# Kernel tuning notes

Measured on AMD Instinct MI355X. Metric: run time of the kernel, lower is better.

The kernel has to match this reference:

```python
import jax, jax.numpy as jnp
import numpy as np

BS, C, H, W = 8, 64, 256, 256
N_MODE_1, N_MODE_2 = 32, 32  # retained modes along H-rfft and W-rfft


def setup_inputs() -> dict:
    key = jax.random.key(0)
    ks = jax.random.split(key, 5)
    ci = co = C // 2
    scale = 1.0 / (C * C)  # module's self.scale flavor; kaiming init approximated by scaled normal
    return {
        "x": jax.random.normal(ks[0], (BS, C, H, W), jnp.float32),
        "w1_re": jax.random.normal(ks[1], (2, ci, co, N_MODE_1), jnp.float32) * 0.05,
        "w1_im": jax.random.normal(ks[2], (2, ci, co, N_MODE_1), jnp.float32) * 0.05,
        "w2_re": jax.random.normal(ks[3], (2, ci, co, N_MODE_2), jnp.float32) * 0.05,
        "w2_im": jax.random.normal(ks[4], (2, ci, co, N_MODE_2), jnp.float32) * 0.05,
    }


def reference(x, w1_re, w1_im, w2_re, w2_im):
    bs, c, h, w = x.shape
    x5 = x.reshape(bs, 2, c // 2, h, w)  # split channels into 2 groups

    # ---- spectral conv along W (dim=-1), weight_2 ----
    w2c = w2_re + 1j * w2_im  # [2, ci, co, n_mode_2]
    x_ft = jnp.fft.rfft(x5, axis=-1, norm="ortho")  # [bs,2,ci,h,w//2+1]
    out_ft = jnp.einsum("bgixy,gioy->bgoxy", x_ft[..., :N_MODE_2], w2c)
    out_ft = jnp.pad(out_ft, ((0, 0), (0, 0), (0, 0), (0, 0), (0, x_ft.shape[-1] - N_MODE_2)))
    x5 = jnp.fft.irfft(out_ft, n=w, axis=-1, norm="ortho")

    # ---- spectral conv along H (dim=-2), weight_1 ----
    w1c = w1_re + 1j * w1_im  # [2, ci, co, n_mode_1]
    x_ft = jnp.fft.rfft(x5, axis=-2, norm="ortho")  # [bs,2,ci,h//2+1,w]
    out_ft = jnp.einsum("bgixy,giox->bgoxy", x_ft[..., :N_MODE_1, :], w1c)
    out_ft = jnp.pad(out_ft, ((0, 0), (0, 0), (0, 0), (0, x_ft.shape[-2] - N_MODE_1), (0, 0)))
    x5 = jnp.fft.irfft(out_ft, n=h, axis=-2, norm="ortho")

    return x5.reshape(bs, c, h, w)
```

## Files before the change

### kernel.cpp

```cpp
#include <hip/hip_runtime.h>
#include <math.h>

#define PI2_256 0.0245436926061702596754894014318f
#define AS 264

typedef __attribute__((ext_vector_type(8))) short short8;
typedef __attribute__((ext_vector_type(4))) float f32x4;

static __device__ __forceinline__ unsigned short f2bf(float f) {
    unsigned int u = __float_as_uint(f);
    u = (u + 0x7FFFu + ((u >> 16) & 1u)) >> 16;
    return (unsigned short)u;
}
static __device__ __forceinline__ float bf2f(unsigned short h) {
    return __uint_as_float(((unsigned int)h) << 16);
}

__global__ __launch_bounds__(256) void init_tab(float* __restrict__ tc, float* __restrict__ ts) {
    int idx = blockIdx.x * 256 + threadIdx.x;
    int k = idx >> 8, n = idx & 255;
    int m = (k * n) & 255;
    float s, c;
    sincosf(PI2_256 * (float)m, &s, &c);
    tc[idx] = c;
    ts[idx] = s;
}

__global__ __launch_bounds__(256) void init_et(unsigned short* __restrict__ Eth,
                                               unsigned short* __restrict__ Etl) {
    int idx = blockIdx.x * 256 + threadIdx.x;
    int n = idx >> 8, w = idx & 255;
    int k = n & 31;
    int m = (k * w) & 255;
    float s, c;
    sincosf(PI2_256 * (float)m, &s, &c);
    float v = (n < 32) ? c : -s;
    unsigned short h = f2bf(v);
    Eth[idx] = h;
    Etl[idx] = f2bf(v - bf2f(h));
}

__global__ __launch_bounds__(256) void w_fwd(const float* __restrict__ x,
                                             const float* __restrict__ w2r,
                                             const float* __restrict__ w2i,
                                             const unsigned short* __restrict__ Eth,
                                             const unsigned short* __restrict__ Etl,
                                             float* __restrict__ Yw) {
    __shared__ __attribute__((aligned(16))) unsigned short Ah[32 * AS];
    __shared__ float XrL[2][32 * 36], XiL[2][32 * 36];

    const int bid = blockIdx.x;
    const int jr  = bid & 127;
    const int g   = (bid >> 7) & 1;
    const int b   = bid >> 8;
    const int t   = threadIdx.x;

    const size_t chan0 = (size_t)(b * 64 + g * 32);

    for (int rr = 0; rr < 2; ++rr) {
        const int xrow = jr * 2 + rr;
        const size_t base = (chan0 * 256 + xrow) * 256;

        {
            const int wq = t & 63, i0 = t >> 6;
            #pragma unroll
            for (int r = 0; r < 8; ++r) {
                const int i = i0 + r * 4;
                const float4 v = *(const float4*)(x + base + (size_t)i * 65536 + wq * 4);
                ushort4 hq;
                hq.x = f2bf(v.x);
                hq.y = f2bf(v.y);
                hq.z = f2bf(v.z);
                hq.w = f2bf(v.w);
                *(ushort4*)(Ah + i * AS + wq * 4) = hq;
            }
        }
        __syncthreads();

        {
            const int l  = t & 63, wv = t >> 6;
            const int lr = l & 15, lk = (l >> 4) * 8;
            f32x4 acc0 = {0.f, 0.f, 0.f, 0.f};
            f32x4 acc1 = {0.f, 0.f, 0.f, 0.f};
            const unsigned short* bhp = Eth + (size_t)(wv * 16 + lr) * 256 + lk;
            const unsigned short* blp = Etl + (size_t)(wv * 16 + lr) * 256 + lk;
            const unsigned short* a0p = Ah + lr * AS + lk;
            const unsigned short* a1p = Ah + (16 + lr) * AS + lk;
            #pragma unroll
            for (int ks = 0; ks < 8; ++ks) {
                const int offg = ks * 32;
                const short8 bh = *(const short8*)(bhp + offg);
                const short8 bl = *(const short8*)(blp + offg);
                const short8 a0 = *(const short8*)(a0p + offg);
                const short8 a1 = *(const short8*)(a1p + offg);
                acc0 = __builtin_amdgcn_mfma_f32_16x16x32_bf16(a0, bh, acc0, 0, 0, 0);
                acc1 = __builtin_amdgcn_mfma_f32_16x16x32_bf16(a1, bh, acc1, 0, 0, 0);
                acc0 = __builtin_amdgcn_mfma_f32_16x16x32_bf16(a0, bl, acc0, 0, 0, 0);
                acc1 = __builtin_amdgcn_mfma_f32_16x16x32_bf16(a1, bl, acc1, 0, 0, 0);
            }
            const int col   = wv * 16 + lr;
            const int rbase = (l >> 4) * 4;
            #pragma unroll
            for (int r = 0; r < 4; ++r) {
                const int row0 = rbase + r;
                const int row1 = 16 + rbase + r;
                const float v0 = acc0[r], v1 = acc1[r];
                if (col < 32) {
                    XrL[rr][row0 * 36 + col] = v0;
                    XrL[rr][row1 * 36 + col] = v1;
                } else {
                    XiL[rr][row0 * 36 + col - 32] = v0;
                    XiL[rr][row1 * 36 + col - 32] = v1;
                }
            }
        }
        __syncthreads();
    }

    {
        const int kq = t & 7, o = t >> 3;
        const int k4 = kq * 4;
        float4 ar0 = {0,0,0,0}, ai0 = {0,0,0,0};
        float4 ar1 = {0,0,0,0}, ai1 = {0,0,0,0};
        const float* wrb = w2r + (size_t)g * 32768 + o * 32 + k4;
        const float* wib = w2i + (size_t)g * 32768 + o * 32 + k4;
        for (int i = 0; i < 32; ++i) {
            const float4 wr  = *(const float4*)(wrb + i * 1024);
            const float4 wi  = *(const float4*)(wib + i * 1024);
            const float4 xr0 = *(const float4*)(&XrL[0][i * 36 + k4]);
            const float4 xi0 = *(const float4*)(&XiL[0][i * 36 + k4]);
            const float4 xr1 = *(const float4*)(&XrL[1][i * 36 + k4]);
            const float4 xi1 = *(const float4*)(&XiL[1][i * 36 + k4]);
            ar0.x += xr0.x * wr.x - xi0.x * wi.x;  ai0.x += xr0.x * wi.x + xi0.x * wr.x;
            ar0.y += xr0.y * wr.y - xi0.y * wi.y;  ai0.y += xr0.y * wi.y + xi0.y * wr.y;
            ar0.z += xr0.z * wr.z - xi0.z * wi.z;  ai0.z += xr0.z * wi.z + xi0.z * wr.z;
            ar0.w += xr0.w * wr.w - xi0.w * wi.w;  ai0.w += xr0.w * wi.w + xi0.w * wr.w;
            ar1.x += xr1.x * wr.x - xi1.x * wi.x;  ai1.x += xr1.x * wi.x + xi1.x * wr.x;
            ar1.y += xr1.y * wr.y - xi1.y * wi.y;  ai1.y += xr1.y * wi.y + xi1.y * wr.y;
            ar1.z += xr1.z * wr.z - xi1.z * wi.z;  ai1.z += xr1.z * wi.z + xi1.z * wr.z;
            ar1.w += xr1.w * wr.w - xi1.w * wi.w;  ai1.w += xr1.w * wi.w + xi1.w * wr.w;
        }
        const float s2 = 2.f / 256.f, s1 = 1.f / 256.f;
        const float s0 = (k4 == 0) ? s1 : s2;
        float* dst0 = Yw + (size_t)((b * 2 + g) * 32 + o) * 16384
                         + (size_t)(jr * 2) * 64 + k4;
        *(float4*)(dst0)           = make_float4(ar0.x * s0, ar0.y * s2, ar0.z * s2, ar0.w * s2);
        *(float4*)(dst0 + 32)      = make_float4(ai0.x * s0, ai0.y * s2, ai0.z * s2, ai0.w * s2);
        *(float4*)(dst0 + 64)      = make_float4(ar1.x * s0, ar1.y * s2, ar1.z * s2, ar1.w * s2);
        *(float4*)(dst0 + 64 + 32) = make_float4(ai1.x * s0, ai1.y * s2, ai1.z * s2, ai1.w * s2);
    }
}

__global__ __launch_bounds__(256) void h_fwd(const float* __restrict__ Yw,
                                             float* __restrict__ Z) {
    __shared__ float YL[256 * 64];
    __shared__ float kC[32], kS[32];
    const int bid = blockIdx.x;
    const int t = threadIdx.x;
    if (t < 32) {
        float s, c; sincosf(PI2_256 * (float)t, &s, &c);
        kC[t] = c; kS[t] = s;
    }
    {
        const float* src = Yw + (size_t)bid * 16384;
        #pragma unroll
        for (int r = 0; r < 16; ++r) {
            const int f = t + r * 256;
            *(float4*)(YL + f * 4) = *(const float4*)(src + f * 4);
        }
    }
    __syncthreads();

    const int hs = t & 1, kg = (t >> 1) & 7, sp = t >> 4;
    const int hb = hs * 64;
    const float sgn = (kg & 1) ? -1.f : 1.f;
    const float4 y0q   = *(const float4*)(YL + sp * 4);
    const float4 y128q = *(const float4*)(YL + 128 * 64 + sp * 4);

    float cA[4], sA[4], cB[4], sB[4], t2[4];
    float xr[4][4], xi[4][4];
    #pragma unroll
    for (int kk = 0; kk < 4; ++kk) {
        const int k = kg + 8 * kk;
        const float cd = kC[k], sd = kS[k];
        t2[kk] = 2.f * cd;
        float cA0, sA0;
        if (hs == 0) { cA0 = 1.f; sA0 = 0.f; }
        else {
            const int km = k & 3;
            cA0 = (km == 0) ? 1.f : (km == 2) ? -1.f : 0.f;
            sA0 = (km == 1) ? 1.f : (km == 3) ? -1.f : 0.f;
        }
        cA[kk] = cA0; sA[kk] = sA0;
        cB[kk] = cA0 * cd + sA0 * sd;
        sB[kk] = sA0 * cd - cA0 * sd;
        #pragma unroll
        for (int j = 0; j < 4; ++j) {
            xr[kk][j] = (hs == 0) ? (sgn * (&y128q.x)[j] - (&y0q.x)[j]) : 0.f;
            xi[kk][j] = 0.f;
        }
    }
    for (int h = hb; h < hb + 64; ++h) {
        const float4 aq = *(const float4*)(YL + h * 64 + sp * 4);
        const float4 mq = *(const float4*)(YL + ((256 - h) & 255) * 64 + sp * 4);
        float ye[4], yo[4];
        #pragma unroll
        for (int j = 0; j < 4; ++j) {
            ye[j] = (&aq.x)[j] + (&mq.x)[j];
            yo[j] = (&aq.x)[j] - (&mq.x)[j];
        }
        #pragma unroll
        for (int kk = 0; kk < 4; ++kk) {
            #pragma unroll
            for (int j = 0; j < 4; ++j) {
                xr[kk][j] += ye[j] * cA[kk];
                xi[kk][j] -= yo[j] * sA[kk];
            }
            const float cn = t2[kk] * cA[kk] - cB[kk]; cB[kk] = cA[kk]; cA[kk] = cn;
            const float sn = t2[kk] * sA[kk] - sB[kk]; sB[kk] = sA[kk]; sA[kk] = sn;
        }
    }
    #pragma unroll
    for (int kk = 0; kk < 4; ++kk)
        #pragma unroll
        for (int j = 0; j < 4; ++j) {
            xr[kk][j] += __shfl_xor(xr[kk][j], 1);
            xi[kk][j] += __shfl_xor(xi[kk][j], 1);
        }
    if (hs == 0) {
        const int o = bid & 31, bg = bid >> 5;
        #pragma unroll
        for (int kk = 0; kk < 4; ++kk) {
            const int k = kg + 8 * kk;
            const size_t zi_ = (((size_t)bg * 32 + k) * 32 + o) * 128 + sp * 4;
            *(float4*)(Z + zi_)      = make_float4(xr[kk][0], xr[kk][1], xr[kk][2], xr[kk][3]);
            *(float4*)(Z + zi_ + 64) = make_float4(xi[kk][0], xi[kk][1], xi[kk][2], xi[kk][3]);
        }
    }
}

__global__ __launch_bounds__(256) void h_mix2(const float* __restrict__ Z,
                                              const float* __restrict__ w1r,
                                              const float* __restrict__ w1i,
                                              float* __restrict__ Z2) {
    __shared__ float ZL[32 * 128];
    __shared__ float WrL[1024], WiL[1024];
    const int bid = blockIdx.x;
    const int kh = bid & 31, bg = bid >> 5;
    const int g = bg & 1;
    const int t = threadIdx.x;
    {
        const float* src = Z + (size_t)bid * 4096;
        #pragma unroll
        for (int r = 0; r < 4; ++r) {
            const int f = t + r * 256;
            *(float4*)(ZL + f * 4) = *(const float4*)(src + f * 4);
        }
        #pragma unroll
        for (int r = 0; r < 4; ++r) {
            const int idx = t + r * 256;
            const int gidx = g * 32768 + (idx >> 5) * 1024 + (idx & 31) * 32 + kh;
            WrL[idx] = w1r[gidx];
            WiL[idx] = w1i[gidx];
        }
    }
    __syncthreads();

    const int s = t & 63, og = t >> 6;
    float accr[8], acci[8];
    #pragma unroll
    for (int m = 0; m < 8; ++m) { accr[m] = 0.f; acci[m] = 0.f; }
    for (int i = 0; i < 32; ++i) {
        const float zr = ZL[i * 128 + s];
        const float zi = ZL[i * 128 + 64 + s];
        #pragma unroll
        for (int m = 0; m < 8; ++m) {
            const int o = og * 8 + m;
            const float wr = WrL[i * 32 + o];
            const float wi = WiL[i * 32 + o];
            accr[m] += zr * wr - zi * wi;
            acci[m] += zr * wi + zi * wr;
        }
    }
    const float sck = (kh == 0) ? (1.f / 256.f) : (2.f / 256.f);
    #pragma unroll
    for (int m = 0; m < 8; ++m) {
        const int o = og * 8 + m;
        const size_t zo = ((size_t)(bg * 32 + o) * 32 + kh) * 128 + s;
        Z2[zo]      = accr[m] * sck;
        Z2[zo + 64] = acci[m] * sck;
    }
}

__global__ __launch_bounds__(256) void h_inv2(const float* __restrict__ Z2,
                                              const float* __restrict__ tc,
                                              const float* __restrict__ ts,
                                              float* __restrict__ YHg) {
    __shared__ float ZL[32 * 128];
    __shared__ float TcL[32 * 128], TsL[32 * 128];
    const int bid = blockIdx.x;
    const int t = threadIdx.x;
    {
        const float* src = Z2 + (size_t)bid * 4096;
        #pragma unroll
        for (int r = 0; r < 4; ++r) {
            const int f = t + r * 256;
            *(float4*)(ZL + f * 4) = *(const float4*)(src + f * 4);
        }
        #pragma unroll
        for (int r = 0; r < 4; ++r) {
            const int q = t + r * 256;
            const int k = q >> 5, hq = q & 31;
            *(float4*)(TcL + k * 128 + hq * 4) = *(const float4*)(tc + (size_t)k * 256 + hq * 4);
            *(float4*)(TsL + k * 128 + hq * 4) = *(const float4*)(ts + (size_t)k * 256 + hq * 4);
        }
    }
    __syncthreads();

    const int s = t & 63, hg = t >> 6;
    float zr[32], zi[32];
    #pragma unroll
    for (int k = 0; k < 32; ++k) {
        zr[k] = ZL[k * 128 + s];
        zi[k] = ZL[k * 128 + 64 + s];
    }
    float* dst = YHg + (size_t)bid * 16384;
    #pragma unroll
    for (int jq = 0; jq < 8; ++jq) {
        const int h0 = hg * 32 + jq * 4;
        float sC[4] = {0, 0, 0, 0}, sS[4] = {0, 0, 0, 0};
        #pragma unroll
        for (int k = 0; k < 32; ++k) {
            const float4 c4 = *(const float4*)(TcL + k * 128 + h0);
            const float4 s4 = *(const float4*)(TsL + k * 128 + h0);
            sC[0] += zr[k] * c4.x;  sS[0] += zi[k] * s4.x;
            sC[1] += zr[k] * c4.y;  sS[1] += zi[k] * s4.y;
            sC[2] += zr[k] * c4.z;  sS[2] += zi[k] * s4.z;
            sC[3] += zr[k] * c4.w;  sS[3] += zi[k] * s4.w;
        }
        #pragma unroll
        for (int jj = 0; jj < 4; ++jj) {
            const int h = h0 + jj;
            dst[h * 64 + s] = sC[jj] - sS[jj];
            if (h > 0) dst[(256 - h) * 64 + s] = sC[jj] + sS[jj];
        }
    }
    if (hg == 0) {
        float ny = 0.f;
        #pragma unroll
        for (int k = 0; k < 32; ++k) ny += (k & 1) ? -zr[k] : zr[k];
        dst[128 * 64 + s] = ny;
    }
}

__global__ __launch_bounds__(256) void w_inv2(const float* __restrict__ YHg,
                                              const float* __restrict__ tc,
                                              const float* __restrict__ ts,
                                              float* __restrict__ out) {
    __shared__ float YL[32 * 64];
    __shared__ float TcL[32 * 128], TsL[32 * 128];
    const int bid = blockIdx.x;
    const int hb = bid & 7, c = bid >> 3;
    const int t = threadIdx.x;
    {
        const float* src = YHg + (size_t)c * 16384 + hb * 2048;
        #pragma unroll
        for (int r = 0; r < 2; ++r) {
            const int f = t + r * 256;
            *(float4*)(YL + f * 4) = *(const float4*)(src + f * 4);
        }
        #pragma unroll
        for (int r = 0; r < 4; ++r) {
            const int q = t + r * 256;
            const int k = q >> 5, wq_ = q & 31;
            *(float4*)(TcL + k * 128 + wq_ * 4) = *(const float4*)(tc + (size_t)k * 256 + wq_ * 4);
            *(float4*)(TsL + k * 128 + wq_ * 4) = *(const float4*)(ts + (size_t)k * 256 + wq_ * 4);
        }
    }
    __syncthreads();

    const int wq = t & 31, hh = t >> 5;
    const int w0 = wq * 4;
    float* outp = out + (size_t)c * 65536;

    float sC[4][4], sS[4][4];
    float nyA[4];
    #pragma unroll
    for (int j = 0; j < 4; ++j) {
        nyA[j] = 0.f;
        #pragma unroll
        for (int jj = 0; jj < 4; ++jj) { sC[j][jj] = 0.f; sS[j][jj] = 0.f; }
    }

    for (int k = 0; k < 32; ++k) {
        const float4 c4 = *(const float4*)(TcL + k * 128 + w0);
        const float4 s4 = *(const float4*)(TsL + k * 128 + w0);
        const float sk = (k & 1) ? -1.f : 1.f;
        #pragma unroll
        for (int j = 0; j < 4; ++j) {
            const int hl = hh * 4 + j;
            const float R = YL[hl * 64 + k];
            const float I = YL[hl * 64 + 32 + k];
            nyA[j] += sk * R;
            sC[j][0] += R * c4.x;  sS[j][0] += I * s4.x;
            sC[j][1] += R * c4.y;  sS[j][1] += I * s4.y;
            sC[j][2] += R * c4.z;  sS[j][2] += I * s4.z;
            sC[j][3] += R * c4.w;  sS[j][3] += I * s4.w;
        }
    }
    #pragma unroll
    for (int j = 0; j < 4; ++j) {
        const int h = hb * 32 + hh * 4 + j;
        *(float4*)(outp + (size_t)h * 256 + w0) =
            make_float4(sC[j][0] - sS[j][0], sC[j][1] - sS[j][1],
                        sC[j][2] - sS[j][2], sC[j][3] - sS[j][3]);
        const float p0 = sC[j][0] + sS[j][0];
        const float p1 = sC[j][1] + sS[j][1];
        const float p2 = sC[j][2] + sS[j][2];
        const float p3 = sC[j][3] + sS[j][3];
        const float m0s = __shfl(p0, 32 - wq, 32);
        const float m0  = (wq == 0) ? nyA[j] : m0s;
        const float m1  = __shfl(p3, 31 - wq, 32);
        const float m2  = __shfl(p2, 31 - wq, 32);
        const float m3  = __shfl(p1, 31 - wq, 32);
        *(float4*)(outp + (size_t)h * 256 + 128 + w0) = make_float4(m0, m1, m2, m3);
    }
}

extern "C" void kernel_launch(void* const* d_in, const int* in_sizes, int n_in,
                              void* d_out, int out_size, void* d_ws, size_t ws_size,
                              hipStream_t stream) {
    const float* x   = (const float*)d_in[0];
    const float* w1r = (const float*)d_in[1];
    const float* w1i = (const float*)d_in[2];
    const float* w2r = (const float*)d_in[3];
    const float* w2i = (const float*)d_in[4];
    float* out = (float*)d_out;
    float* ws  = (float*)d_ws;

    float* tc = ws;
    float* ts = ws + 8192;
    float* Yw = ws + 16384;
    float* Z  = Yw + 8388608;
    float* Z2 = Z + 2097152;
    unsigned short* Eth = (unsigned short*)(Z2 + 2097152);
    unsigned short* Etl = Eth + 16384;

    init_tab<<<32, 256, 0, stream>>>(tc, ts);
    init_et<<<64, 256, 0, stream>>>(Eth, Etl);
    w_fwd<<<2048, 256, 0, stream>>>(x, w2r, w2i, Eth, Etl, Yw);
    h_fwd<<<512, 256, 0, stream>>>(Yw, Z);
    h_mix2<<<512, 256, 0, stream>>>(Z, w1r, w1i, Z2);
    h_inv2<<<512, 256, 0, stream>>>(Z2, tc, ts, Yw);
    w_inv2<<<4096, 256, 0, stream>>>(Yw, tc, ts, out);
}
```

Before: 176.6 us.

## Split W-axis forward DFT and channel mixing into separate kernels via bf16 intermediate

The fused w_fwd kernel, which computed the truncated W-axis DFT for two rows and then mixed channels, is split into two kernels. w_dft runs one row per block across 4096 blocks and writes the retained spectrum as bf16 to scratch that aliases Z. w_mix reads that scratch back and performs the complex channel mixing. The aim is more parallelism and less serialised work per block in the MFMA stage, at the cost of an extra launch, an extra global round trip, and an added bf16 rounding of the spectral coefficients.

Result: slower. 188.9 us (+7.0%).

```diff
diff --git a/kernel.cpp b/kernel.cpp
--- a/kernel.cpp
+++ b/kernel.cpp
@@ -5,6 +5,7 @@
 #define AS 264
 
 typedef __attribute__((ext_vector_type(8))) short short8;
+typedef __attribute__((ext_vector_type(8))) unsigned short ushort8;
 typedef __attribute__((ext_vector_type(4))) float f32x4;
 
 static __device__ __forceinline__ unsigned short f2bf(float f) {
@@ -40,14 +41,94 @@
     Etl[idx] = f2bf(v - bf2f(h));
 }
 
-__global__ __launch_bounds__(256) void w_fwd(const float* __restrict__ x,
+__global__ __launch_bounds__(256) void w_dft(const float* __restrict__ x,
+                                             const unsigned short* __restrict__ Eth,
+                                             const unsigned short* __restrict__ Etl,
+                                             unsigned short* __restrict__ Xg) {
+    __shared__ __attribute__((aligned(16))) unsigned short Ah[32 * AS];
+    __shared__ float XrL[32 * 36], XiL[32 * 36];
+
+    const int bid  = blockIdx.x;
+    const int xrow = bid & 255;
+    const int g    = (bid >> 8) & 1;
+    const int b    = bid >> 9;
+    const int t    = threadIdx.x;
+
+    const size_t chan0 = (size_t)(b * 64 + g * 32);
+    const size_t base  = (chan0 * 256 + xrow) * 256;
+
+    {
+        const int wq = t & 63, i0 = t >> 6;
+        #pragma unroll
+        for (int r = 0; r < 8; ++r) {
+            const int i = i0 + r * 4;
+            const float4 v = *(const float4*)(x + base + (size_t)i * 65536 + wq * 4);
+            ushort4 hq;
+            hq.x = f2bf(v.x);
+            hq.y = f2bf(v.y);
+            hq.z = f2bf(v.z);
+            hq.w = f2bf(v.w);
+            *(ushort4*)(Ah + i * AS + wq * 4) = hq;
+        }
+    }
+    __syncthreads();
+
+    {
+        const int l  = t & 63, wv = t >> 6;
+        const int lr = l & 15, lk = (l >> 4) * 8;
+        f32x4 acc0 = {0.f, 0.f, 0.f, 0.f};
+        f32x4 acc1 = {0.f, 0.f, 0.f, 0.f};
+        const unsigned short* bhp = Eth + (size_t)(wv * 16 + lr) * 256 + lk;
+        const unsigned short* blp = Etl + (size_t)(wv * 16 + lr) * 256 + lk;
+        const unsigned short* a0p = Ah + lr * AS + lk;
+        const unsigned short* a1p = Ah + (16 + lr) * AS + lk;
+        #pragma unroll
+        for (int ks = 0; ks < 8; ++ks) {
+            const int offg = ks * 32;
+            const short8 bh = *(const short8*)(bhp + offg);
+            const short8 bl = *(const short8*)(blp + offg);
+            const short8 a0 = *(const short8*)(a0p + offg);
+            const short8 a1 = *(const short8*)(a1p + offg);
+            acc0 = __builtin_amdgcn_mfma_f32_16x16x32_bf16(a0, bh, acc0, 0, 0, 0);
+            acc1 = __builtin_amdgcn_mfma_f32_16x16x32_bf16(a1, bh, acc1, 0, 0, 0);
+            acc0 = __builtin_amdgcn_mfma_f32_16x16x32_bf16(a0, bl, acc0, 0, 0, 0);
+            acc1 = __builtin_amdgcn_mfma_f32_16x16x32_bf16(a1, bl, acc1, 0, 0, 0);
+        }
+        const int col   = wv * 16 + lr;
+        const int rbase = (l >> 4) * 4;
+        #pragma unroll
+        for (int r = 0; r < 4; ++r) {
+            const int row0 = rbase + r;
+            const int row1 = 16 + rbase + r;
+            const float v0 = acc0[r], v1 = acc1[r];
+            if (col < 32) {
+                XrL[row0 * 36 + col] = v0;
+                XrL[row1 * 36 + col] = v1;
+            } else {
+                XiL[row0 * 36 + col - 32] = v0;
+                XiL[row1 * 36 + col - 32] = v1;
+            }
+        }
+    }
+    __syncthreads();
+
+    {
+        const int i = t >> 3, q = t & 7;
+        const float* srcL = ((q < 4) ? XrL : XiL) + i * 36 + (q & 3) * 8;
+        const float4 u0 = *(const float4*)(srcL);
+        const float4 u1 = *(const float4*)(srcL + 4);
+        ushort8 hv;
+        hv[0] = f2bf(u0.x); hv[1] = f2bf(u0.y); hv[2] = f2bf(u0.z); hv[3] = f2bf(u0.w);
+        hv[4] = f2bf(u1.x); hv[5] = f2bf(u1.y); hv[6] = f2bf(u1.z); hv[7] = f2bf(u1.w);
+        *(ushort8*)(Xg + (chan0 + i) * 16384 + (size_t)xrow * 64 + q * 8) = hv;
+    }
+}
+
+__global__ __launch_bounds__(256) void w_mix(const unsigned short* __restrict__ Xg,
                                              const float* __restrict__ w2r,
                                              const float* __restrict__ w2i,
-                                             const unsigned short* __restrict__ Eth,
-                                             const unsigned short* __restrict__ Etl,
                                              float* __restrict__ Yw) {
-    __shared__ __attribute__((aligned(16))) unsigned short Ah[32 * AS];
-    __shared__ float XrL[2][32 * 36], XiL[2][32 * 36];
+    __shared__ float XL[2][32 * 64];
 
     const int bid = blockIdx.x;
     const int jr  = bid & 127;
@@ -57,65 +138,18 @@
 
     const size_t chan0 = (size_t)(b * 64 + g * 32);
 
-    for (int rr = 0; rr < 2; ++rr) {
-        const int xrow = jr * 2 + rr;
-        const size_t base = (chan0 * 256 + xrow) * 256;
-
-        {
-            const int wq = t & 63, i0 = t >> 6;
-            #pragma unroll
-            for (int r = 0; r < 8; ++r) {
-                const int i = i0 + r * 4;
-                const float4 v = *(const float4*)(x + base + (size_t)i * 65536 + wq * 4);
-                ushort4 hq;
-                hq.x = f2bf(v.x);
-                hq.y = f2bf(v.y);
-                hq.z = f2bf(v.z);
-                hq.w = f2bf(v.w);
-                *(ushort4*)(Ah + i * AS + wq * 4) = hq;
-            }
-        }
-        __syncthreads();
-
-        {
-            const int l  = t & 63, wv = t >> 6;
-            const int lr = l & 15, lk = (l >> 4) * 8;
-            f32x4 acc0 = {0.f, 0.f, 0.f, 0.f};
-            f32x4 acc1 = {0.f, 0.f, 0.f, 0.f};
-            const unsigned short* bhp = Eth + (size_t)(wv * 16 + lr) * 256 + lk;
-            const unsigned short* blp = Etl + (size_t)(wv * 16 + lr) * 256 + lk;
-            const unsigned short* a0p = Ah + lr * AS + lk;
-            const unsigned short* a1p = Ah + (16 + lr) * AS + lk;
-            #pragma unroll
-            for (int ks = 0; ks < 8; ++ks) {
-                const int offg = ks * 32;
-                const short8 bh = *(const short8*)(bhp + offg);
-                const short8 bl = *(const short8*)(blp + offg);
-                const short8 a0 = *(const short8*)(a0p + offg);
-                const short8 a1 = *(const short8*)(a1p + offg);
-                acc0 = __builtin_amdgcn_mfma_f32_16x16x32_bf16(a0, bh, acc0, 0, 0, 0);
-                acc1 = __builtin_amdgcn_mfma_f32_16x16x32_bf16(a1, bh, acc1, 0, 0, 0);
-                acc0 = __builtin_amdgcn_mfma_f32_16x16x32_bf16(a0, bl, acc0, 0, 0, 0);
-                acc1 = __builtin_amdgcn_mfma_f32_16x16x32_bf16(a1, bl, acc1, 0, 0, 0);
-            }
-            const int col   = wv * 16 + lr;
-            const int rbase = (l >> 4) * 4;
-            #pragma unroll
-            for (int r = 0; r < 4; ++r) {
-                const int row0 = rbase + r;
-                const int row1 = 16 + rbase + r;
-                const float v0 = acc0[r], v1 = acc1[r];
-                if (col < 32) {
-                    XrL[rr][row0 * 36 + col] = v0;
-                    XrL[rr][row1 * 36 + col] = v1;
-                } else {
-                    XiL[rr][row0 * 36 + col - 32] = v0;
-                    XiL[rr][row1 * 36 + col - 32] = v1;
-                }
-            }
-        }
-        __syncthreads();
-    }
+    #pragma unroll
+    for (int r = 0; r < 2; ++r) {
+        const int idx = t + r * 256;
+        const int c = idx >> 4, rem = idx & 15;
+        const int row = rem >> 3, q = rem & 7;
+        const ushort8 hv = *(const ushort8*)(Xg + (chan0 + c) * 16384
+                                             + (size_t)(jr * 2 + row) * 64 + q * 8);
+        float* dst = &XL[row][c * 64 + q * 8];
+        dst[0] = bf2f(hv[0]); dst[1] = bf2f(hv[1]); dst[2] = bf2f(hv[2]); dst[3] = bf2f(hv[3]);
+        dst[4] = bf2f(hv[4]); dst[5] = bf2f(hv[5]); dst[6] = bf2f(hv[6]); dst[7] = bf2f(hv[7]);
+    }
+    __syncthreads();
 
     {
         const int kq = t & 7, o = t >> 3;
@@ -127,10 +161,10 @@
         for (int i = 0; i < 32; ++i) {
             const float4 wr  = *(const float4*)(wrb + i * 1024);
             const float4 wi  = *(const float4*)(wib + i * 1024);
-            const float4 xr0 = *(const float4*)(&XrL[0][i * 36 + k4]);
-            const float4 xi0 = *(const float4*)(&XiL[0][i * 36 + k4]);
-            const float4 xr1 = *(const float4*)(&XrL[1][i * 36 + k4]);
-            const float4 xi1 = *(const float4*)(&XiL[1][i * 36 + k4]);
+            const float4 xr0 = *(const float4*)(&XL[0][i * 64 + k4]);
+            const float4 xi0 = *(const float4*)(&XL[0][i * 64 + 32 + k4]);
+            const float4 xr1 = *(const float4*)(&XL[1][i * 64 + k4]);
+            const float4 xi1 = *(const float4*)(&XL[1][i * 64 + 32 + k4]);
             ar0.x += xr0.x * wr.x - xi0.x * wi.x;  ai0.x += xr0.x * wi.x + xi0.x * wr.x;
             ar0.y += xr0.y * wr.y - xi0.y * wi.y;  ai0.y += xr0.y * wi.y + xi0.y * wr.y;
             ar0.z += xr0.z * wr.z - xi0.z * wi.z;  ai0.z += xr0.z * wi.z + xi0.z * wr.z;
@@ -445,10 +479,12 @@
     float* Z2 = Z + 2097152;
     unsigned short* Eth = (unsigned short*)(Z2 + 2097152);
     unsigned short* Etl = Eth + 16384;
+    unsigned short* Xg = (unsigned short*)Z;
 
     init_tab<<<32, 256, 0, stream>>>(tc, ts);
     init_et<<<64, 256, 0, stream>>>(Eth, Etl);
-    w_fwd<<<2048, 256, 0, stream>>>(x, w2r, w2i, Eth, Etl, Yw);
+    w_dft<<<4096, 256, 0, stream>>>(x, Eth, Etl, Xg);
+    w_mix<<<2048, 256, 0, stream>>>(Xg, w2r, w2i, Yw);
     h_fwd<<<512, 256, 0, stream>>>(Yw, Z);
     h_mix2<<<512, 256, 0, stream>>>(Z, w1r, w1i, Z2);
     h_inv2<<<512, 256, 0, stream>>>(Z2, tc, ts, Yw);
```
